# Kernel tuning notes

Measured on AMD Instinct MI355X. Metric: run time of the kernel, lower is better.

Reference implementation:

```python
import jax, jax.numpy as jnp
import numpy as np
import math

H = 2048          # hidden_size
NH = 16           # num_attn_heads
HD = H // NH      # attn head dim = 128
NFW = 4           # num_lact_heads
FD = H // NFW     # fw head dim = 512
DH = FD           # inter_multi = 1.0
CHUNK = 512       # lact_chunk_size
WINDOW = 2048     # window_size
ROPE_BASE = 500000.0
BASE_LR_INV = math.log(math.expm1(0.001))  # inv_softplus(1e-3)


def rmsnorm(x, w, eps=1e-6):
    return x * jax.lax.rsqrt(jnp.mean(x * x, axis=-1, keepdims=True) + eps) * w


def l2norm(x, eps=1e-12):
    return x * jax.lax.rsqrt(jnp.sum(x * x, axis=-1, keepdims=True) + eps)


def rope(x):  # x: [b, h, s, d], half-split convention
    d = x.shape[-1]
    s = x.shape[2]
    inv = 1.0 / (ROPE_BASE ** (jnp.arange(d // 2, dtype=jnp.float32) / (d // 2)))
    f = jnp.arange(s, dtype=jnp.float32)[:, None] * inv[None, :]  # [s, d/2]
    cos, sin = jnp.cos(f), jnp.sin(f)
    x1, x2 = x[..., : d // 2], x[..., d // 2:]
    return jnp.concatenate([x1 * cos - x2 * sin, x2 * cos + x1 * sin], axis=-1)


def setup_inputs() -> dict:
    key = jax.random.key(0)
    ks = jax.random.split(key, 8)
    b, s = 2, 2048
    return {
        "hidden_states": jax.random.normal(ks[0], (b, s, H), jnp.float32),
        "qkv_w": jax.random.normal(ks[1], (3 * H, H), jnp.float32) / math.sqrt(H),
        "q_norm_w": jnp.ones((H,), jnp.float32),
        "k_norm_w": jnp.ones((H,), jnp.float32),
        "qk_scale": jnp.ones((H, 2), jnp.float32),
        "qk_offset": jnp.zeros((H, 2), jnp.float32),
        "lr_w": jax.random.normal(ks[2], (3 * NFW, H), jnp.float32) / math.sqrt(H),
        "lr_b": jnp.zeros((3 * NFW,), jnp.float32),
        "w0": jax.random.normal(ks[3], (NFW, DH, FD), jnp.float32) / math.sqrt(FD),
        "w1": jax.random.normal(ks[4], (NFW, FD, DH), jnp.float32) / math.sqrt(DH),
        "w2": jax.random.normal(ks[5], (NFW, DH, FD), jnp.float32) / math.sqrt(FD),
        "ttt_norm_w": jnp.ones((FD,), jnp.float32),
        "o_proj_w": jax.random.normal(ks[6], (H, H), jnp.float32) / math.sqrt(H),
    }


def reference(hidden_states, qkv_w, q_norm_w, k_norm_w, qk_scale, qk_offset,
              lr_w, lr_b, w0, w1, w2, ttt_norm_w, o_proj_w):
    x = hidden_states
    b, s, _ = x.shape
    nc = s // CHUNK

    qkv = x @ qkv_w.T
    q, k, v = jnp.split(qkv, 3, axis=-1)
    q = rmsnorm(q, q_norm_w)
    k = rmsnorm(k, k_norm_w)

    # ---- TTT (fast-weight SwiGLU) branch ----
    fq = jax.nn.silu(q * qk_scale[:, 0] + qk_offset[:, 0])
    fk = jax.nn.silu(k * qk_scale[:, 1] + qk_offset[:, 1])
    fv = jax.nn.silu(v)
    tohead = lambda t: t.reshape(b, s, NFW, FD).transpose(0, 2, 1, 3)  # [b,h,s,d]
    fq, fk, fv = l2norm(tohead(fq)), l2norm(tohead(fk)), tohead(fv)

    lr = jax.nn.softplus(x @ lr_w.T + lr_b + BASE_LR_INV)          # [b,s,3*NFW]
    lr = lr.reshape(b, s, 3, NFW).transpose(2, 0, 3, 1)[..., None]  # [3,b,h,s,1]
    lr0, lr1, lr2 = lr[0], lr[1], lr[2]

    chunkify = lambda t: t.reshape(b, NFW, nc, CHUNK, -1).transpose(2, 0, 1, 3, 4)
    qs, ks_, vs = chunkify(fq), chunkify(fk), chunkify(fv)
    l0s, l1s, l2s = chunkify(lr0), chunkify(lr1), chunkify(lr2)

    w0b = jnp.broadcast_to(w0, (b,) + w0.shape)
    w1b = jnp.broadcast_to(w1, (b,) + w1.shape)
    w2b = jnp.broadcast_to(w2, (b,) + w2.shape)

    def step(carry, xs):
        w0c, w1c, w2c = carry
        qc, kc, vc, l0, l1, l2 = xs
        # apply current fast weights to queries (strictly causal across chunks)
        hq = jax.nn.silu(jnp.einsum('bhcd,bhed->bhce', qc, w0c)) * \
             jnp.einsum('bhcd,bhed->bhce', qc, w2c)
        oc = jnp.einsum('bhce,bhde->bhcd', hq, w1c)
        # gradient-descent update on dot-product loss -sum(v * f(k))
        g1 = jnp.einsum('bhcd,bhed->bhce', kc, w0c)
        g2 = jnp.einsum('bhcd,bhed->bhce', kc, w2c)
        gate = jax.nn.silu(g1)
        hidden = gate * g2
        dhidden = jnp.einsum('bhcd,bhde->bhce', vc, w1c)  # w1^T v
        dh2 = dhidden * gate
        sig = jax.nn.sigmoid(g1)
        dh1 = dhidden * g2 * (sig * (1.0 + g1 * (1.0 - sig)))  # silu'(g1)
        w1n = w1c + jnp.einsum('bhcd,bhce->bhde', l1 * vc, hidden)
        w0n = w0c + jnp.einsum('bhce,bhcd->bhed', l0 * dh1, kc)
        w2n = w2c + jnp.einsum('bhce,bhcd->bhed', l2 * dh2, kc)
        return (w0n, w1n, w2n), oc

    _, o_chunks = jax.lax.scan(step, (w0b, w1b, w2b), (qs, ks_, vs, l0s, l1s, l2s))
    o_ttt = o_chunks.transpose(1, 2, 0, 3, 4).reshape(b, NFW, s, FD)
    o_ttt = rmsnorm(o_ttt, ttt_norm_w)
    o_ttt = o_ttt.transpose(0, 2, 1, 3).reshape(b, s, H)

    # ---- sliding-window attention branch ----
    qa = rope(q.reshape(b, s, NH, HD).transpose(0, 2, 1, 3))
    ka = rope(k.reshape(b, s, NH, HD).transpose(0, 2, 1, 3))
    va = v.reshape(b, s, NH, HD).transpose(0, 2, 1, 3)
    scores = jnp.einsum('bhqd,bhkd->bhqk', qa, ka) / math.sqrt(HD)
    i = jnp.arange(s)
    mask = (i[:, None] >= i[None, :]) & (i[:, None] - i[None, :] < WINDOW)
    scores = jnp.where(mask, scores, jnp.float32(-1e9))
    p = jax.nn.softmax(scores, axis=-1)
    attn = jnp.einsum('bhqk,bhkd->bhqd', p, va).transpose(0, 2, 1, 3).reshape(b, s, H)

    return (attn + o_ttt) @ o_proj_w.T
```

## Files before the change

kernel.cpp:

```cpp
#include <hip/hip_runtime.h>
#include <hip/hip_bf16.h>
#include <math.h>

using bf16 = __hip_bfloat16;

namespace {

constexpr int cH = 2048;
constexpr int cNH = 16;
constexpr int cHD = 128;
constexpr int cNFW = 4;
constexpr int cFD = 512;
constexpr int cS = 2048;
constexpr float cRSQRT_HD = 0.08838834764831845f;
constexpr long ZL_ = 262144;
constexpr long ZG_ = 1048576;

typedef __attribute__((ext_vector_type(8))) short short8;
typedef __attribute__((ext_vector_type(4))) float f32x4;

__device__ __forceinline__ float sigmoidf_(float x) { return 1.0f / (1.0f + __expf(-x)); }
__device__ __forceinline__ float b2f(bf16 v) { return __bfloat162float(v); }
__device__ __forceinline__ bf16 f2b(float v) { return __float2bfloat16(v); }
__device__ __forceinline__ unsigned short f2bu(float f) {
  return __builtin_bit_cast(unsigned short, __float2bfloat16(f));
}
__device__ __forceinline__ float bu2f(unsigned u) { return __uint_as_float(u << 16); }

#if defined(__has_builtin)
#if __has_builtin(__builtin_amdgcn_global_load_lds)
#define HAVE_GLOAD 1
#endif
#endif

__device__ __forceinline__ void gload16(const bf16* g, short* ldsbase) {
#ifdef HAVE_GLOAD
  __builtin_amdgcn_global_load_lds((const __attribute__((address_space(1))) void*)g,
                                   (__attribute__((address_space(3))) void*)ldsbase, 16, 0, 0);
#else
  const int l = threadIdx.x & 63;
  *(uint4*)(ldsbase + l * 8) = *(const uint4*)g;
#endif
}

__device__ __forceinline__ void stage16(const bf16* src, short* dst) {
  *(uint4*)dst = *(const uint4*)src;
  *(uint4*)(dst + 8) = *(const uint4*)(src + 8);
}

__device__ __forceinline__ void store1(float* p, float v) { *p = v; }
__device__ __forceinline__ void store1(bf16* p, float v) { *p = f2b(v); }

__device__ __forceinline__ void mm_core32(const bf16* __restrict__ Ab, int lda,
                                          const bf16* __restrict__ Bb, int ldb, int K,
                                          short* As, short* Bs, f32x4 acc[4][4]) {
  const int t = threadIdx.x, lane = t & 63, g = lane >> 4, c16 = lane & 15;
  const int wv = t >> 6, wm = (wv >> 1) * 64, wn = (wv & 1) * 64;
  for (int k0 = 0; k0 < K; k0 += 32) {
    __syncthreads();
    {
      const int ch = wv * 2;
      const bf16* ga = Ab + (size_t)(ch * 16 + (lane >> 2)) * lda + k0 + (lane & 3) * 8;
      gload16(ga, &As[ch * 512]);
      gload16(ga + (size_t)16 * lda, &As[ch * 512 + 512]);
      const bf16* gb = Bb + (size_t)(ch * 16 + (lane >> 2)) * ldb + k0 + (lane & 3) * 8;
      gload16(gb, &Bs[ch * 512]);
      gload16(gb + (size_t)16 * ldb, &Bs[ch * 512 + 512]);
    }
    __syncthreads();
    short8 af[4], bfr[4];
#pragma unroll
    for (int mi = 0; mi < 4; ++mi) af[mi] = *(const short8*)&As[(wm + mi * 16 + c16) * 32 + g * 8];
#pragma unroll
    for (int ni = 0; ni < 4; ++ni) bfr[ni] = *(const short8*)&Bs[(wn + ni * 16 + c16) * 32 + g * 8];
#pragma unroll
    for (int mi = 0; mi < 4; ++mi)
#pragma unroll
      for (int ni = 0; ni < 4; ++ni)
        acc[mi][ni] = __builtin_amdgcn_mfma_f32_16x16x32_bf16(af[mi], bfr[ni], acc[mi][ni], 0, 0, 0);
  }
}

template <bool ACC, bool MIR, typename TC>
__device__ __forceinline__ void mm_store(TC* Cb, bf16* Mb, int ldc, int rb, int cb, f32x4 acc[4][4]) {
  const int t = threadIdx.x, lane = t & 63, g = lane >> 4, c16 = lane & 15;
  const int wv = t >> 6, wm = (wv >> 1) * 64, wn = (wv & 1) * 64;
  const int rbase = rb + wm, cbase = cb + wn;
#pragma unroll
  for (int mi = 0; mi < 4; ++mi)
#pragma unroll
    for (int ni = 0; ni < 4; ++ni) {
      const int col = cbase + ni * 16 + c16;
#pragma unroll
      for (int r = 0; r < 4; ++r) {
        const int row = rbase + mi * 16 + g * 4 + r;
        TC* cp = Cb + (size_t)row * ldc + col;
        if constexpr (ACC) {
          float nv = *cp + acc[mi][ni][r];
          *cp = nv;
          if constexpr (MIR) Mb[(size_t)row * ldc + col] = f2b(nv);
        } else {
          store1(cp, acc[mi][ni][r]);
        }
      }
    }
}

template <typename TC>
__global__ __launch_bounds__(256) void k_mm(const bf16* __restrict__ A, int lda,
                                            const bf16* __restrict__ B, int ldb,
                                            TC* __restrict__ C, int ldc, int K) {
  __shared__ short As[128 * 32];
  __shared__ short Bs[128 * 32];
  const bf16* Ab = A + (size_t)blockIdx.y * 128 * lda;
  const bf16* Bb = B + (size_t)blockIdx.x * 128 * ldb;
  f32x4 acc[4][4];
  const f32x4 zero4 = {0.f, 0.f, 0.f, 0.f};
#pragma unroll
  for (int i = 0; i < 4; ++i)
#pragma unroll
    for (int j = 0; j < 4; ++j) acc[i][j] = zero4;
  mm_core32(Ab, lda, Bb, ldb, K, As, Bs, acc);
  mm_store<false, false>(C, (bf16*)nullptr, ldc, blockIdx.y * 128, blockIdx.x * 128, acc);
}

__global__ __launch_bounds__(256) void k_fuse1(const bf16* __restrict__ fq, const bf16* __restrict__ fk,
                                               const bf16* __restrict__ fv,
                                               const bf16* __restrict__ w0b, const bf16* __restrict__ w1t,
                                               const bf16* __restrict__ w2b,
                                               bf16* __restrict__ hq, bf16* __restrict__ trH,
                                               bf16* __restrict__ trD1, bf16* __restrict__ trD2,
                                               bf16* __restrict__ trK, bf16* __restrict__ trV,
                                               const float* __restrict__ lr0, const float* __restrict__ lr1,
                                               const float* __restrict__ lr2,
                                               const bf16* __restrict__ occ,
                                               const float* __restrict__ tw, bf16* __restrict__ y,
                                               int chunk) {
  __shared__ short S[12288];
  __shared__ float red[4];
  const int id = blockIdx.x, t = threadIdx.x;
  const size_t choff = (size_t)chunk * 262144;

  if (id < 512) {
    const int bh = id >> 6, tile = id & 63, by = tile >> 3, bx = tile & 7;
    const int lane = t & 63, g = lane >> 4, c16 = lane & 15, wv = t >> 6;
    const int wm = (wv >> 1) * 32, wn = (wv & 1) * 32;
    const bf16* Aq = fq + (size_t)bh * ZG_ + choff + (size_t)(by * 64) * cFD;
    const bf16* Ak = fk + (size_t)bh * ZG_ + choff + (size_t)(by * 64) * cFD;
    const bf16* Av = fv + (size_t)bh * ZG_ + choff + (size_t)(by * 64) * cFD;
    const bf16* B0 = w0b + (size_t)bh * ZL_ + (size_t)(bx * 64) * cFD;
    const bf16* B2 = w2b + (size_t)bh * ZL_ + (size_t)(bx * 64) * cFD;
    const bf16* B1 = w1t + (size_t)bh * ZL_ + (size_t)(bx * 64) * cFD;

    f32x4 acc[5][2][2];
    const f32x4 zero4 = {0.f, 0.f, 0.f, 0.f};
#pragma unroll
    for (int v = 0; v < 5; ++v)
#pragma unroll
      for (int i = 0; i < 2; ++i)
#pragma unroll
        for (int j = 0; j < 2; ++j) acc[v][i][j] = zero4;

    const int srow = wv * 16 + (lane >> 2), scol = (lane & 3) * 8;
    for (int k0 = 0; k0 < 512; k0 += 32) {
      __syncthreads();
      gload16(Aq + (size_t)srow * cFD + k0 + scol, &S[0 + wv * 512]);
      gload16(Ak + (size_t)srow * cFD + k0 + scol, &S[2048 + wv * 512]);
      gload16(Av + (size_t)srow * cFD + k0 + scol, &S[4096 + wv * 512]);
      gload16(B0 + (size_t)srow * cFD + k0 + scol, &S[6144 + wv * 512]);
      gload16(B2 + (size_t)srow * cFD + k0 + scol, &S[8192 + wv * 512]);
      gload16(B1 + (size_t)srow * cFD + k0 + scol, &S[10240 + wv * 512]);
      __syncthreads();
      short8 aq[2], ak[2], av[2], b0[2], b2[2], b1[2];
#pragma unroll
      for (int mi = 0; mi < 2; ++mi) {
        const int ro = (wm + mi * 16 + c16) * 32 + g * 8;
        aq[mi] = *(const short8*)&S[0 + ro];
        ak[mi] = *(const short8*)&S[2048 + ro];
        av[mi] = *(const short8*)&S[4096 + ro];
      }
#pragma unroll
      for (int ni = 0; ni < 2; ++ni) {
        const int ro = (wn + ni * 16 + c16) * 32 + g * 8;
        b0[ni] = *(const short8*)&S[6144 + ro];
        b2[ni] = *(const short8*)&S[8192 + ro];
        b1[ni] = *(const short8*)&S[10240 + ro];
      }
#pragma unroll
      for (int mi = 0; mi < 2; ++mi)
#pragma unroll
        for (int ni = 0; ni < 2; ++ni) {
          acc[0][mi][ni] = __builtin_amdgcn_mfma_f32_16x16x32_bf16(aq[mi], b0[ni], acc[0][mi][ni], 0, 0, 0);
          acc[1][mi][ni] = __builtin_amdgcn_mfma_f32_16x16x32_bf16(aq[mi], b2[ni], acc[1][mi][ni], 0, 0, 0);
          acc[2][mi][ni] = __builtin_amdgcn_mfma_f32_16x16x32_bf16(ak[mi], b0[ni], acc[2][mi][ni], 0, 0, 0);
          acc[3][mi][ni] = __builtin_amdgcn_mfma_f32_16x16x32_bf16(ak[mi], b2[ni], acc[3][mi][ni], 0, 0, 0);
          acc[4][mi][ni] = __builtin_amdgcn_mfma_f32_16x16x32_bf16(av[mi], b1[ni], acc[4][mi][ni], 0, 0, 0);
        }
    }

    float l0v[2][4], l2v[2][4];
#pragma unroll
    for (int mi = 0; mi < 2; ++mi)
#pragma unroll
      for (int r = 0; r < 4; ++r) {
        const int row = by * 64 + wm + mi * 16 + g * 4 + r;
        l0v[mi][r] = lr0[bh * 2048 + chunk * 512 + row];
        l2v[mi][r] = lr2[bh * 2048 + chunk * 512 + row];
      }
#pragma unroll
    for (int mi = 0; mi < 2; ++mi)
#pragma unroll
      for (int ni = 0; ni < 2; ++ni)
#pragma unroll
        for (int r = 0; r < 4; ++r) {
          float hq1 = acc[0][mi][ni][r], hq2 = acc[1][mi][ni][r];
          float g1 = acc[2][mi][ni][r], g2 = acc[3][mi][ni][r], dh = acc[4][mi][ni][r];
          acc[0][mi][ni][r] = hq1 * sigmoidf_(hq1) * hq2;
          float sg = sigmoidf_(g1);
          float gate = g1 * sg;
          acc[1][mi][ni][r] = gate * g2;
          acc[2][mi][ni][r] = l0v[mi][r] * dh * g2 * (sg * (1.0f + g1 * (1.0f - sg)));
          acc[3][mi][ni][r] = l2v[mi][r] * dh * gate;
        }

    short* Ts = S;
    bf16* dst0 = hq + (size_t)bh * ZL_;
    bf16* dstT[3] = {trH + (size_t)bh * ZL_, trD1 + (size_t)bh * ZL_, trD2 + (size_t)bh * ZL_};
#pragma unroll
    for (int rd = 0; rd < 4; ++rd) {
      __syncthreads();
#pragma unroll
      for (int mi = 0; mi < 2; ++mi)
#pragma unroll
        for (int ni = 0; ni < 2; ++ni)
#pragma unroll
          for (int r = 0; r < 4; ++r) {
            const int row = wm + mi * 16 + g * 4 + r, col = wn + ni * 16 + c16;
            if (rd == 0) Ts[row * 66 + col] = (short)f2bu(acc[0][mi][ni][r]);
            else Ts[col * 66 + row] = (short)f2bu(acc[rd][mi][ni][r]);
          }
      __syncthreads();
      const int rr = t >> 2, cs = (t & 3) * 16;
      unsigned short u[16] __attribute__((aligned(16)));
#pragma unroll
      for (int i = 0; i < 16; ++i) u[i] = (unsigned short)Ts[rr * 66 + cs + i];
      bf16* dp = (rd == 0) ? (dst0 + (size_t)(by * 64 + rr) * cFD + bx * 64 + cs)
                           : (dstT[rd - 1] + (size_t)(bx * 64 + rr) * cFD + by * 64 + cs);
      *(uint4*)dp = *(uint4*)u;
      *(uint4*)(dp + 8) = *(uint4*)(u + 8);
    }
  } else if (id < 1536) {
    short* Ts = S;
    const int id2 = id - 512;
    const int var = id2 >> 9, bh = (id2 >> 6) & 7, by = (id2 >> 3) & 7, bx = id2 & 7;
    const bf16* src = ((var == 0) ? fk : fv) + choff + (size_t)bh * ZG_;
    bf16* dst = ((var == 0) ? trK : trV) + (size_t)bh * ZL_;
    {
      const int rr = t >> 2, cseg = (t & 3) * 16;
      if (var == 0) {
        stage16(src + (size_t)(by * 64 + rr) * cFD + bx * 64 + cseg, &Ts[rr * 72 + cseg]);
      } else {
        const float s = lr1[bh * 2048 + chunk * 512 + by * 64 + rr];
        const bf16* p = src + (size_t)(by * 64 + rr) * cFD + bx * 64 + cseg;
        unsigned short u[16] __attribute__((aligned(16)));
#pragma unroll
        for (int i = 0; i < 16; ++i) u[i] = f2bu(b2f(p[i]) * s);
        *(uint4*)&Ts[rr * 72 + cseg] = *(uint4*)u;
        *(uint4*)&Ts[rr * 72 + cseg + 8] = *(uint4*)(u + 8);
      }
    }
    __syncthreads();
    {
      const int oc_ = t >> 2, rseg = (t & 3) * 16;
      unsigned short u[16] __attribute__((aligned(16)));
#pragma unroll
      for (int i = 0; i < 16; ++i) u[i] = (unsigned short)Ts[(rseg + i) * 72 + oc_];
      bf16* dp = dst + (size_t)(bx * 64 + oc_) * cFD + by * 64 + rseg;
      *(uint4*)dp = *(uint4*)u;
      *(uint4*)(dp + 8) = *(uint4*)(u + 8);
    }
  } else {
    const int rrow = id - 1536;
    const int bh = rrow >> 9, rr = rrow & 511;
    const bf16* src = occ + ((size_t)bh * 512 + rr) * 512;
    float v0 = b2f(src[t]), v1 = b2f(src[t + 256]);
    float ss = v0 * v0 + v1 * v1;
    for (int d = 32; d; d >>= 1) ss += __shfl_down(ss, d);
    if ((t & 63) == 0) red[t >> 6] = ss;
    __syncthreads();
    const float rstd = rsqrtf((red[0] + red[1] + red[2] + red[3]) / cFD + 1e-6f);
    const int si = (chunk - 1) * 512 + rr;
    bf16* dst = y + ((size_t)((bh >> 2) * cS) + si) * cH + (bh & 3) * cFD;
    dst[t] = f2b(b2f(dst[t]) + v0 * rstd * tw[t]);
    dst[t + 256] = f2b(b2f(dst[t + 256]) + v1 * rstd * tw[t + 256]);
  }
}

__global__ __launch_bounds__(256) void k_updna(const bf16* __restrict__ trV, const bf16* __restrict__ trH,
                                               const bf16* __restrict__ trD1, const bf16* __restrict__ trD2,
                                               const bf16* __restrict__ trK,
                                               const bf16* __restrict__ hq, const bf16* __restrict__ w1bc,
                                               float* w0s, float* w1s, float* w2s,
                                               bf16* w0b, bf16* w1bn, bf16* w2b, bf16* w1t,
                                               bf16* __restrict__ occ) {
  __shared__ short Sh[8704];
  const int id = blockIdx.x, t = threadIdx.x;
  const int lane = t & 63, g = lane >> 4, c16 = lane & 15, wv = t >> 6;
  if (id < 384) {
    short* As = Sh;
    short* Bs = Sh + 4096;
    const int z = id >> 4, tile = id & 15, by = tile >> 2, bx = tile & 3;
    const int var = z >> 3, bh = z & 7;
    const bf16 *Aa, *Bb;
    if (var == 0) {
      Aa = trV + (size_t)bh * ZL_ + (size_t)by * 128 * cFD;
      Bb = trH + (size_t)bh * ZL_ + (size_t)bx * 128 * cFD;
    } else if (var == 1) {
      Aa = trD1 + (size_t)bh * ZL_ + (size_t)by * 128 * cFD;
      Bb = trK + (size_t)bh * ZL_ + (size_t)bx * 128 * cFD;
    } else {
      Aa = trD2 + (size_t)bh * ZL_ + (size_t)by * 128 * cFD;
      Bb = trK + (size_t)bh * ZL_ + (size_t)bx * 128 * cFD;
    }
    f32x4 acc[4][4];
    const f32x4 zero4 = {0.f, 0.f, 0.f, 0.f};
#pragma unroll
    for (int i = 0; i < 4; ++i)
#pragma unroll
      for (int j = 0; j < 4; ++j) acc[i][j] = zero4;
    mm_core32(Aa, cFD, Bb, cFD, cFD, As, Bs, acc);
    if (var == 1) {
      mm_store<true, true>(w0s + (size_t)bh * ZL_, w0b + (size_t)bh * ZL_, cFD, by * 128, bx * 128, acc);
    } else if (var == 2) {
      mm_store<true, true>(w2s + (size_t)bh * ZL_, w2b + (size_t)bh * ZL_, cFD, by * 128, bx * 128, acc);
    } else {
      float* W = w1s + (size_t)bh * ZL_;
      bf16* M = w1bn + (size_t)bh * ZL_;
      const int wm = (wv >> 1) * 64, wn = (wv & 1) * 64;
#pragma unroll
      for (int mi = 0; mi < 4; ++mi)
#pragma unroll
        for (int ni = 0; ni < 4; ++ni) {
          const int col = bx * 128 + wn + ni * 16 + c16;
#pragma unroll
          for (int r = 0; r < 4; ++r) {
            const int row = by * 128 + wm + mi * 16 + g * 4 + r;
            float nv = W[(size_t)row * cFD + col] + acc[mi][ni][r];
            W[(size_t)row * cFD + col] = nv;
            M[(size_t)row * cFD + col] = f2b(nv);
            acc[mi][ni][r] = nv;
          }
        }
      bf16* T = w1t + (size_t)bh * ZL_;
      short* Ts = Sh;
#pragma unroll
      for (int rd = 0; rd < 2; ++rd) {
        __syncthreads();
        if (wn == rd * 64) {
#pragma unroll
          for (int mi = 0; mi < 4; ++mi)
#pragma unroll
            for (int ni = 0; ni < 4; ++ni) {
              const int cc = ni * 16 + c16;
              unsigned short u[4] __attribute__((aligned(8)));
#pragma unroll
              for (int r = 0; r < 4; ++r) u[r] = f2bu(acc[mi][ni][r]);
              *(uint2*)&Ts[cc * 136 + wm + mi * 16 + g * 4] = *(uint2*)u;
            }
        }
        __syncthreads();
        const int cc = t >> 2, seg = (t & 3) * 32;
        unsigned short u[32] __attribute__((aligned(16)));
#pragma unroll
        for (int i = 0; i < 32; ++i) u[i] = (unsigned short)Ts[cc * 136 + seg + i];
        bf16* dp = T + (size_t)(bx * 128 + rd * 64 + cc) * cFD + by * 128 + seg;
        *(uint4*)dp = *(uint4*)u;
        *(uint4*)(dp + 8) = *(uint4*)(u + 8);
        *(uint4*)(dp + 16) = *(uint4*)(u + 16);
        *(uint4*)(dp + 24) = *(uint4*)(u + 24);
      }
    }
  } else {
    short* As = Sh;
    short* Bs = Sh + 4096;
    const int id2 = id - 384;
    const int bh = id2 >> 4, tile = id2 & 15, by = tile >> 2, bx = tile & 3;
    const bf16* Aa = hq + (size_t)bh * ZL_ + (size_t)by * 128 * cFD;
    const bf16* Bb = w1bc + (size_t)bh * ZL_ + (size_t)bx * 128 * cFD;
    f32x4 acc[4][4];
    const f32x4 zero4 = {0.f, 0.f, 0.f, 0.f};
#pragma unroll
    for (int i = 0; i < 4; ++i)
#pragma unroll
      for (int j = 0; j < 4; ++j) acc[i][j] = zero4;
    mm_core32(Aa, cFD, Bb, cFD, cFD, As, Bs, acc);
    mm_store<false, false>(occ + (size_t)bh * ZL_, (bf16*)nullptr, cFD, by * 128, bx * 128, acc);
  }
}

__global__ __launch_bounds__(256) void k_normcvt(const bf16* __restrict__ occ,
                                                 const float* __restrict__ tw, bf16* __restrict__ y,
                                                 const float* __restrict__ opw, bf16* __restrict__ opwb,
                                                 int chunk) {
  __shared__ float red[4];
  const int id = blockIdx.x, t = threadIdx.x;
  if (id < 4096) {
    const int bh = id >> 9, rr = id & 511;
    const bf16* src = occ + ((size_t)bh * 512 + rr) * 512;
    float v0 = b2f(src[t]), v1 = b2f(src[t + 256]);
    float ss = v0 * v0 + v1 * v1;
    for (int d = 32; d; d >>= 1) ss += __shfl_down(ss, d);
    if ((t & 63) == 0) red[t >> 6] = ss;
    __syncthreads();
    const float rstd = rsqrtf((red[0] + red[1] + red[2] + red[3]) / cFD + 1e-6f);
    const int si = chunk * 512 + rr;
    bf16* dst = y + ((size_t)((bh >> 2) * cS) + si) * cH + (bh & 3) * cFD;
    dst[t] = f2b(b2f(dst[t]) + v0 * rstd * tw[t]);
    dst[t + 256] = f2b(b2f(dst[t + 256]) + v1 * rstd * tw[t + 256]);
  } else {
    const size_t i = ((size_t)(id - 4096) * 256 + t) * 8;
    float4 a = *(const float4*)(opw + i), b = *(const float4*)(opw + i + 4);
    unsigned short u[8] __attribute__((aligned(16)));
    u[0] = f2bu(a.x); u[1] = f2bu(a.y); u[2] = f2bu(a.z); u[3] = f2bu(a.w);
    u[4] = f2bu(b.x); u[5] = f2bu(b.y); u[6] = f2bu(b.z); u[7] = f2bu(b.w);
    *(uint4*)(opwb + i) = *(uint4*)u;
  }
}

__global__ __launch_bounds__(256) void k_prep(const float* __restrict__ x, const float* __restrict__ qkv_w,
                                              const float* __restrict__ w0, const float* __restrict__ w1,
                                              const float* __restrict__ w2,
                                              const float* __restrict__ lr_w, const float* __restrict__ lr_b,
                                              bf16* __restrict__ xb, bf16* __restrict__ qkvwb,
                                              float* __restrict__ w0s, float* __restrict__ w1s,
                                              float* __restrict__ w2s,
                                              float* __restrict__ ct, float* __restrict__ stb,
                                              float* lr0, float* lr1, float* lr2, float base) {
  __shared__ float xbuf[cH];
  const int id = blockIdx.x, t = threadIdx.x;
  if (id < 4096) {
    const size_t i = ((size_t)id * 256 + t) * 8;
    float4 a = *(const float4*)(x + i), b = *(const float4*)(x + i + 4);
    unsigned short u[8] __attribute__((aligned(16)));
    u[0] = f2bu(a.x); u[1] = f2bu(a.y); u[2] = f2bu(a.z); u[3] = f2bu(a.w);
    u[4] = f2bu(b.x); u[5] = f2bu(b.y); u[6] = f2bu(b.z); u[7] = f2bu(b.w);
    *(uint4*)(xb + i) = *(uint4*)u;
  } else if (id < 10240) {
    const size_t i = ((size_t)(id - 4096) * 256 + t) * 8;
    float4 a = *(const float4*)(qkv_w + i), b = *(const float4*)(qkv_w + i + 4);
    unsigned short u[8] __attribute__((aligned(16)));
    u[0] = f2bu(a.x); u[1] = f2bu(a.y); u[2] = f2bu(a.z); u[3] = f2bu(a.w);
    u[4] = f2bu(b.x); u[5] = f2bu(b.y); u[6] = f2bu(b.z); u[7] = f2bu(b.w);
    *(uint4*)(qkvwb + i) = *(uint4*)u;
  } else if (id < 16384) {
    const int sub = id - 10240;
    const int w = sub >> 11, blk = sub & 2047;
    const size_t i = ((size_t)blk * 256 + t) * 4;
    const int f = (int)((i >> 18) & 3);
    const size_t off = i & 262143;
    const float* src = (w == 0) ? w0 : (w == 1) ? w1 : w2;
    float* dst = (w == 0) ? w0s : (w == 1) ? w1s : w2s;
    *(float4*)(dst + i) = *(const float4*)(src + (size_t)f * 262144 + off);
  } else if (id < 16896) {
    const int gid = (id - 16384) * 256 + t;
    const int si = gid >> 6, jj = gid & 63;
    float inv = powf(500000.0f, -(float)jj / 64.0f);
    float ang = (float)si * inv;
    ct[(size_t)si * 64 + jj] = cosf(ang);
    stb[(size_t)si * 64 + jj] = sinf(ang);
  } else {
    const int token = id - 16896, b_ = token >> 11, si = token & 2047;
    const int wv = t >> 6, lane = t & 63;
    const float* xr = x + (size_t)token * cH;
    for (int i = t; i < cH; i += 256) xbuf[i] = xr[i];
    __syncthreads();
#pragma unroll
    for (int jj = 0; jj < 3; ++jj) {
      const int j = wv * 3 + jj;
      const float* wr = lr_w + (size_t)j * cH;
      float s = 0.f;
      for (int k = lane; k < cH; k += 64) s += xbuf[k] * wr[k];
      for (int d = 32; d; d >>= 1) s += __shfl_down(s, d);
      if (lane == 0) {
        float v = s + lr_b[j] + base;
        float sp = (v > 15.f) ? v : log1pf(expf(v));
        const int tt = j >> 2, f = j & 3;
        float* dst = (tt == 0 ? lr0 : tt == 1 ? lr1 : lr2);
        dst[(size_t)(b_ * cNFW + f) * cS + si] = sp;
      }
    }
  }
}

__global__ __launch_bounds__(256) void k_post2(bf16* __restrict__ qkvh,
                                               const float* __restrict__ qnw, const float* __restrict__ knw,
                                               const float* __restrict__ ct, const float* __restrict__ stb,
                                               bf16* __restrict__ qa, bf16* __restrict__ ka,
                                               bf16* __restrict__ vt) {
  __shared__ short smem[8704];
  __shared__ float red[4];
  const int id = blockIdx.x, t = threadIdx.x;
  if (id < 4096) {
    float* buf = (float*)smem;
    const int token = id, b_ = token >> 11, si = token & 2047;
    bf16* base = qkvh + (size_t)token * 3 * cH;
    for (int pass = 0; pass < 2; ++pass) {
      __syncthreads();
      bf16* src = base + pass * cH;
      const float* nw = pass ? knw : qnw;
      float ss = 0.f;
      for (int i = t; i < cH; i += 256) {
        float v = b2f(src[i]);
        buf[i] = v;
        ss += v * v;
      }
      for (int d = 32; d; d >>= 1) ss += __shfl_down(ss, d);
      if ((t & 63) == 0) red[t >> 6] = ss;
      __syncthreads();
      const float rstd = rsqrtf((red[0] + red[1] + red[2] + red[3]) / cH + 1e-6f);
      for (int i = t; i < cH; i += 256) {
        float v = buf[i] * rstd * nw[i];
        buf[i] = v;
        src[i] = f2b(v);
      }
      __syncthreads();
      bf16* dst = pass ? ka : qa;
      const float scale = pass ? 1.f : cRSQRT_HD;
      const int hh = t >> 4, j0 = (t & 15) * 4;
      const float* cr = ct + (size_t)si * 64 + j0;
      const float* sr = stb + (size_t)si * 64 + j0;
      bf16* drow = dst + ((size_t)(b_ * cNH + hh) * cS + si) * cHD;
      unsigned short u1[4] __attribute__((aligned(8))), u2[4] __attribute__((aligned(8)));
#pragma unroll
      for (int i = 0; i < 4; ++i) {
        float x1 = buf[hh * cHD + j0 + i], x2 = buf[hh * cHD + 64 + j0 + i];
        u1[i] = f2bu((x1 * cr[i] - x2 * sr[i]) * scale);
        u2[i] = f2bu((x2 * cr[i] + x1 * sr[i]) * scale);
      }
      *(uint2*)(drow + j0) = *(uint2*)u1;
      *(uint2*)(drow + 64 + j0) = *(uint2*)u2;
    }
  } else {
    short* Ts = smem;
    const int id2 = id - 4096;
    const int tile = id2 & 31, h = (id2 >> 5) & 15, b_ = id2 >> 9;
    {
      const int r = t >> 2, seg = (t & 3) * 32;
      const bf16* src = qkvh + ((size_t)(b_ * cS) + tile * 64 + r) * 3 * cH + 2 * cH + h * cHD + seg;
      stage16(src, &Ts[r * 136 + seg]);
      stage16(src + 16, &Ts[r * 136 + seg + 16]);
    }
    __syncthreads();
    {
      const int d = t >> 1, seg2 = (t & 1) * 32;
      unsigned short u[32] __attribute__((aligned(16)));
#pragma unroll
      for (int i = 0; i < 32; ++i) u[i] = (unsigned short)Ts[(seg2 + i) * 136 + d];
      bf16* dp = vt + ((size_t)(b_ * cNH + h) * cHD + d) * cS + tile * 64 + seg2;
      *(uint4*)dp = *(uint4*)u;
      *(uint4*)(dp + 8) = *(uint4*)(u + 8);
      *(uint4*)(dp + 16) = *(uint4*)(u + 16);
      *(uint4*)(dp + 24) = *(uint4*)(u + 24);
    }
  }
}

__global__ __launch_bounds__(256) void k_mid(const bf16* __restrict__ qkvh,
                                             const float* __restrict__ qk_scale,
                                             const float* __restrict__ qk_offset,
                                             bf16* fq, bf16* fk, bf16* fv,
                                             const float* __restrict__ w0s_, bf16* __restrict__ w0b_,
                                             const float* __restrict__ w1s_, bf16* __restrict__ w1t_) {
  __shared__ short Ts[64 * 72];
  const int id = blockIdx.x, t = threadIdx.x;
  if (id < 4096) {
    const int token = id, b_ = token >> 11, si = token & 2047;
    const bf16* base = qkvh + (size_t)token * 3 * cH;
#pragma unroll
    for (int pass = 0; pass < 2; ++pass) {
      const bf16* src = base + pass * cH;
      bf16* fdst = pass ? fk : fq;
      const int head = t >> 6, lane = t & 63;
      float f[8];
      float ss2 = 0.f;
#pragma unroll
      for (int k = 0; k < 8; ++k) {
        const int idx = head * cFD + lane + k * 64;
        float v = b2f(src[idx]);
        float u = v * qk_scale[idx * 2 + pass] + qk_offset[idx * 2 + pass];
        float fv_ = u * sigmoidf_(u);
        f[k] = fv_;
        ss2 += fv_ * fv_;
      }
      for (int d = 1; d < 64; d <<= 1) ss2 += __shfl_xor(ss2, d);
      const float sc2 = rsqrtf(ss2 + 1e-12f);
      bf16* dst = fdst + ((size_t)(b_ * cNFW + head) * cS + si) * cFD;
#pragma unroll
      for (int k = 0; k < 8; ++k) dst[lane + k * 64] = f2b(f[k] * sc2);
    }
    const bf16* vr = base + 2 * cH;
    for (int i = t; i < cH; i += 256) {
      float v = b2f(vr[i]);
      fv[((size_t)(b_ * cNFW + (i >> 9)) * cS + si) * cFD + (i & 511)] = f2b(v * sigmoidf_(v));
    }
  } else if (id < 7168) {
    const size_t i = ((size_t)(id - 4096) * 256 + t) * 8;
    float4 a = *(const float4*)(w0s_ + i), b = *(const float4*)(w0s_ + i + 4);
    unsigned short u[8] __attribute__((aligned(16)));
    u[0] = f2bu(a.x); u[1] = f2bu(a.y); u[2] = f2bu(a.z); u[3] = f2bu(a.w);
    u[4] = f2bu(b.x); u[5] = f2bu(b.y); u[6] = f2bu(b.z); u[7] = f2bu(b.w);
    *(uint4*)(w0b_ + i) = *(uint4*)u;
  } else {
    const int id3 = id - 7168;
    const int bh = id3 >> 6, tile = id3 & 63, by = tile >> 3, bx = tile & 7;
    {
      const int rr = t >> 2, cseg = (t & 3) * 16;
      const float* p = w1s_ + (size_t)bh * ZL_ + (size_t)(by * 64 + rr) * cFD + bx * 64 + cseg;
      unsigned short u[16] __attribute__((aligned(16)));
#pragma unroll
      for (int i = 0; i < 16; ++i) u[i] = f2bu(p[i]);
      *(uint4*)&Ts[rr * 72 + cseg] = *(uint4*)u;
      *(uint4*)&Ts[rr * 72 + cseg + 8] = *(uint4*)(u + 8);
    }
    __syncthreads();
    {
      const int oc_ = t >> 2, rseg = (t & 3) * 16;
      unsigned short u[16] __attribute__((aligned(16)));
#pragma unroll
      for (int i = 0; i < 16; ++i) u[i] = (unsigned short)Ts[(rseg + i) * 72 + oc_];
      bf16* dp = w1t_ + (size_t)bh * ZL_ + (size_t)(bx * 64 + oc_) * cFD + by * 64 + rseg;
      *(uint4*)dp = *(uint4*)u;
      *(uint4*)(dp + 8) = *(uint4*)(u + 8);
    }
  }
}

__global__ __launch_bounds__(512) void k_attn6(const bf16* __restrict__ qa, const bf16* __restrict__ ka,
                                               const bf16* __restrict__ vt, bf16* __restrict__ y) {
  const int id = blockIdx.x;
  const int xcd = id & 7;
  const int j = id >> 3;
  const int p = j & 7;
  const int hb = (j >> 3) * 8 + xcd;
  const int h = hb & 15, b_ = hb >> 4;
  __shared__ short KsP[9216];
  __shared__ short Vts[128 * 72];
  const int t = threadIdx.x, lane = t & 63, g = lane >> 4, c16 = lane & 15, wv = t >> 6;
  const size_t hbq = (size_t)(b_ * cNH + h) * cS;
  const bf16* vb = vt + (size_t)(b_ * cNH + h) * (size_t)(cHD * cS);
  const int r = t >> 3, seg = (t & 7) * 16;
  const int dv = t >> 2, seg2 = (t & 3) * 16;
  const f32x4 zero4 = {0.f, 0.f, 0.f, 0.f};

  for (int half = 0; half < 2; ++half) {
    const int qt = half ? p : 15 - p;
    const int q0 = qt * 128;
    const int nkt = 2 * qt + 2;
    short8 qf[4];
    {
      const bf16* qsrc = qa + (hbq + q0 + wv * 16 + c16) * cHD;
#pragma unroll
      for (int ks = 0; ks < 4; ++ks) qf[ks] = *(const short8*)(qsrc + ks * 32 + g * 8);
    }
    f32x4 o[8];
#pragma unroll
    for (int i = 0; i < 8; ++i) o[i] = zero4;
    float m[4], l[4];
#pragma unroll
    for (int rr = 0; rr < 4; ++rr) { m[rr] = -1e30f; l[rr] = 0.f; }

    uint4 kp0, kp1, vp0, vp1;
    {
      const bf16* ksrc = ka + (hbq + r) * cHD + seg;
      kp0 = *(const uint4*)ksrc; kp1 = *(const uint4*)(ksrc + 8);
      const bf16* vsrc = vb + (size_t)dv * cS + seg2;
      vp0 = *(const uint4*)vsrc; vp1 = *(const uint4*)(vsrc + 8);
    }

    for (int kt = 0; kt < nkt; ++kt) {
      __syncthreads();
      {
        short* kd = &KsP[r * 136 + seg];
        *(uint4*)kd = kp0; *(uint4*)(kd + 8) = kp1;
        short* vd = &Vts[dv * 72 + seg2];
        *(uint4*)vd = vp0; *(uint4*)(vd + 8) = vp1;
      }
      __syncthreads();
      if (kt + 1 < nkt) {
        const bf16* ksrc = ka + (hbq + (kt + 1) * 64 + r) * cHD + seg;
        kp0 = *(const uint4*)ksrc; kp1 = *(const uint4*)(ksrc + 8);
        const bf16* vsrc = vb + (size_t)dv * cS + (kt + 1) * 64 + seg2;
        vp0 = *(const uint4*)vsrc; vp1 = *(const uint4*)(vsrc + 8);
      } else if (half == 0) {
        const bf16* ksrc = ka + (hbq + r) * cHD + seg;
        kp0 = *(const uint4*)ksrc; kp1 = *(const uint4*)(ksrc + 8);
        const bf16* vsrc = vb + (size_t)dv * cS + seg2;
        vp0 = *(const uint4*)vsrc; vp1 = *(const uint4*)(vsrc + 8);
      }

      f32x4 s4[4];
#pragma unroll
      for (int ni = 0; ni < 4; ++ni) s4[ni] = zero4;
      __builtin_amdgcn_s_setprio(1);
#pragma unroll
      for (int ks = 0; ks < 4; ++ks) {
#pragma unroll
        for (int ni = 0; ni < 4; ++ni) {
          short8 bb = *(const short8*)&KsP[(ni * 16 + c16) * 136 + ks * 32 + g * 8];
          s4[ni] = __builtin_amdgcn_mfma_f32_16x16x32_bf16(qf[ks], bb, s4[ni], 0, 0, 0);
        }
      }
      __builtin_amdgcn_s_setprio(0);
      __syncthreads();
      if (kt * 64 + 64 > q0) {
#pragma unroll
        for (int ni = 0; ni < 4; ++ni) {
          const int kv = kt * 64 + ni * 16 + c16;
#pragma unroll
          for (int rr = 0; rr < 4; ++rr) {
            const int qr = q0 + wv * 16 + g * 4 + rr;
            if (kv > qr) s4[ni][rr] = -1e9f;
          }
        }
      }
      float mx[4];
#pragma unroll
      for (int rr = 0; rr < 4; ++rr)
        mx[rr] = fmaxf(fmaxf(s4[0][rr], s4[1][rr]), fmaxf(s4[2][rr], s4[3][rr]));
#pragma unroll
      for (int d = 1; d < 16; d <<= 1)
#pragma unroll
        for (int rr = 0; rr < 4; ++rr) mx[rr] = fmaxf(mx[rr], __shfl_xor(mx[rr], d));
      bool need = false;
#pragma unroll
      for (int rr = 0; rr < 4; ++rr) need |= (mx[rr] > m[rr] + 8.f);
      if (__any(need)) {
        float corr[4];
#pragma unroll
        for (int rr = 0; rr < 4; ++rr) {
          float mn = fmaxf(m[rr], mx[rr]);
          corr[rr] = __expf(m[rr] - mn);
          m[rr] = mn;
        }
#pragma unroll
        for (int rr = 0; rr < 4; ++rr) l[rr] *= corr[rr];
#pragma unroll
        for (int nf = 0; nf < 8; ++nf)
#pragma unroll
          for (int rr = 0; rr < 4; ++rr) o[nf][rr] *= corr[rr];
      }
      float psum[4] = {0.f, 0.f, 0.f, 0.f};
#pragma unroll
      for (int ni = 0; ni < 4; ++ni)
#pragma unroll
        for (int rr = 0; rr < 4; ++rr) {
          float pp = __expf(s4[ni][rr] - m[rr]);
          s4[ni][rr] = pp;
          psum[rr] += pp;
        }
#pragma unroll
      for (int d = 1; d < 16; d <<= 1)
#pragma unroll
        for (int rr = 0; rr < 4; ++rr) psum[rr] += __shfl_xor(psum[rr], d);
#pragma unroll
      for (int rr = 0; rr < 4; ++rr) l[rr] += psum[rr];
      short* pw = &KsP[wv * 1152];
#pragma unroll
      for (int ni = 0; ni < 4; ++ni)
#pragma unroll
        for (int rr = 0; rr < 4; ++rr)
          pw[(g * 4 + rr) * 72 + ni * 16 + c16] = (short)f2bu(s4[ni][rr]);
      __builtin_amdgcn_s_setprio(1);
#pragma unroll
      for (int ks2 = 0; ks2 < 2; ++ks2) {
        short8 a = *(const short8*)&pw[c16 * 72 + ks2 * 32 + g * 8];
#pragma unroll
        for (int nf = 0; nf < 8; ++nf) {
          short8 bb = *(const short8*)&Vts[(nf * 16 + c16) * 72 + ks2 * 32 + g * 8];
          o[nf] = __builtin_amdgcn_mfma_f32_16x16x32_bf16(a, bb, o[nf], 0, 0, 0);
        }
      }
      __builtin_amdgcn_s_setprio(0);
    }
    float inv[4];
#pragma unroll
    for (int rr = 0; rr < 4; ++rr) inv[rr] = 1.f / l[rr];
#pragma unroll
    for (int nf = 0; nf < 8; ++nf)
#pragma unroll
      for (int rr = 0; rr < 4; ++rr) {
        const size_t row = (size_t)(b_ * cS) + q0 + wv * 16 + g * 4 + rr;
        y[row * cH + h * cHD + nf * 16 + c16] = f2b(o[nf][rr] * inv[rr]);
      }
  }
}

}

extern "C" void kernel_launch(void* const* d_in, const int* in_sizes, int n_in,
                              void* d_out, int out_size, void* d_ws, size_t ws_size,
                              hipStream_t stream) {
  (void)in_sizes; (void)n_in; (void)out_size; (void)ws_size;
  const float* x         = (const float*)d_in[0];
  const float* qkv_w     = (const float*)d_in[1];
  const float* q_norm_w  = (const float*)d_in[2];
  const float* k_norm_w  = (const float*)d_in[3];
  const float* qk_scale  = (const float*)d_in[4];
  const float* qk_offset = (const float*)d_in[5];
  const float* lr_w      = (const float*)d_in[6];
  const float* lr_b      = (const float*)d_in[7];
  const float* w0        = (const float*)d_in[8];
  const float* w1        = (const float*)d_in[9];
  const float* w2        = (const float*)d_in[10];
  const float* ttt_nw    = (const float*)d_in[11];
  const float* o_proj_w  = (const float*)d_in[12];
  float* out = (float*)d_out;

  char* Wb = (char*)d_ws;
  bf16* qkvh = (bf16*)Wb;
  bf16* hq   = (bf16*)(Wb + 0UL);
  bf16* trH  = (bf16*)(Wb + 4194304UL);
  bf16* trD1 = (bf16*)(Wb + 8388608UL);
  bf16* trD2 = (bf16*)(Wb + 12582912UL);
  bf16* trK  = (bf16*)(Wb + 16777216UL);
  bf16* trV  = (bf16*)(Wb + 20971520UL);
  bf16* occ  = (bf16*)(Wb + 25165824UL);
  bf16* w1t  = (bf16*)(Wb + 29360128UL);
  bf16* w0b  = (bf16*)(Wb + 33554432UL);
  bf16* w1b0 = (bf16*)(Wb + 37748736UL);
  bf16* w2b  = (bf16*)(Wb + 41943040UL);
  bf16* w1b1 = (bf16*)(Wb + 46137344UL);
  bf16* opwb = (bf16*)(Wb + 0UL);
  size_t off = 50331648UL;
  bf16* fqb = (bf16*)(Wb + off); off += 16777216UL;
  bf16* fkb = (bf16*)(Wb + off); off += 16777216UL;
  bf16* fvb = (bf16*)(Wb + off); off += 16777216UL;
  float* w0s = (float*)(Wb + off); off += 8388608UL;
  float* w1s = (float*)(Wb + off); off += 8388608UL;
  float* w2s = (float*)(Wb + off); off += 8388608UL;
  float* lr0 = (float*)(Wb + off); off += 65536UL;
  float* lr1 = (float*)(Wb + off); off += 65536UL;
  float* lr2 = (float*)(Wb + off); off += 65536UL;
  bf16* y = (bf16*)(Wb + off); off += 16777216UL;
  float* ct  = (float*)(Wb + off); off += 524288UL;
  float* stb = (float*)(Wb + off); off += 524288UL;
  bf16* xb = fqb;
  bf16* qkvwb = fkb;
  bf16* qa = fqb;
  bf16* ka = fkb;
  bf16* vt = fvb;
  bf16* w1m[2] = {w1b0, w1b1};

  const float base_lr_inv = logf(expm1f(0.001f));
  dim3 blk(256);

  k_prep<<<dim3(20992), blk, 0, stream>>>(x, qkv_w, w0, w1, w2, lr_w, lr_b,
                                          xb, qkvwb, w0s, w1s, w2s, ct, stb,
                                          lr0, lr1, lr2, base_lr_inv);
  k_mm<bf16><<<dim3(48, 32), blk, 0, stream>>>(xb, 2048, qkvwb, 2048, qkvh, 6144, 2048);
  k_post2<<<dim3(5120), blk, 0, stream>>>(qkvh, q_norm_w, k_norm_w, ct, stb, qa, ka, vt);
  k_attn6<<<dim3(256), dim3(512), 0, stream>>>(qa, ka, vt, y);
  k_mid<<<dim3(7680), blk, 0, stream>>>(qkvh, qk_scale, qk_offset, fqb, fkb, fvb,
                                        w0s, w0b, w1s, w1t);

  for (int c = 0; c < 4; ++c) {
    const int g1 = (c == 0) ? 1536 : 5632;
    k_fuse1<<<dim3(g1), blk, 0, stream>>>(fqb, fkb, fvb, w0b, w1t, w2b,
                                          hq, trH, trD1, trD2, trK, trV,
                                          lr0, lr1, lr2, occ, ttt_nw, y, c);
    k_updna<<<dim3(512), blk, 0, stream>>>(trV, trH, trD1, trD2, trK, hq, w1m[c & 1],
                                           w0s, w1s, w2s, w0b, w1m[(c + 1) & 1], w2b, w1t,
                                           occ);
  }
  k_normcvt<<<dim3(6144), blk, 0, stream>>>(occ, ttt_nw, y, o_proj_w, opwb, 3);
  k_mm<float><<<dim3(16, 32), blk, 0, stream>>>(y, 2048, opwb, 2048, out, 2048, 2048);
}
```

Measured before the change: 696.4 us.

## Replace GEMM kernel with 256x128 tiled, double-buffered 8-wave MFMA kernel

Replaces the 128x128 single-buffered GEMM used for the QKV and output projections with a 512-thread kernel computing 256x128 tiles. It uses K=64 steps, double-buffered LDS, direct global-to-LDS loads interleaved with MFMA, barriers split per half-tile, and raised wave priority during the MFMA sections. The aim is to hide memory latency and raise per-block data reuse. In exchange it halves the block count (768 and 256 blocks), which may underfill the GPU for the smaller output projection, and the schedule depends on hand-placed waitcnts being correct.

```diff
diff --git a/kernel.cpp b/kernel.cpp
--- a/kernel.cpp
+++ b/kernel.cpp
@@ -107,21 +107,104 @@
 }
 
 template <typename TC>
-__global__ __launch_bounds__(256) void k_mm(const bf16* __restrict__ A, int lda,
-                                            const bf16* __restrict__ B, int ldb,
-                                            TC* __restrict__ C, int ldc, int K) {
-  __shared__ short As[128 * 32];
-  __shared__ short Bs[128 * 32];
-  const bf16* Ab = A + (size_t)blockIdx.y * 128 * lda;
+__global__ __launch_bounds__(512, 1) void k_mm8(const bf16* __restrict__ A, int lda,
+                                                const bf16* __restrict__ B, int ldb,
+                                                TC* __restrict__ C, int ldc, int K) {
+  __shared__ short LA[2][256 * 64];
+  __shared__ short LB[2][128 * 64];
+  const int t = threadIdx.x, lane = t & 63, wv = t >> 6;
+  const int g = lane >> 4, c16 = lane & 15;
+  const int wm = (wv >> 1) * 64, wn = (wv & 1) * 64;
+  const bf16* Ab = A + (size_t)blockIdx.y * 256 * lda;
   const bf16* Bb = B + (size_t)blockIdx.x * 128 * ldb;
+  const int NKT = K >> 6;
+  const int srow = wv * 16 + (lane >> 3), scol = (lane & 7) * 8;
+
+  auto stA = [&](int buf, int half, int kt) {
+    const int ktc = (kt < NKT) ? kt : 0;
+    const bf16* src = Ab + (size_t)(half * 128 + srow) * lda + ktc * 64 + scol;
+    short* dst = &LA[buf][(half * 128 + wv * 16) * 64];
+    gload16(src, dst);
+    gload16(src + (size_t)8 * lda, dst + 512);
+  };
+  auto stB = [&](int buf, int kt) {
+    const int ktc = (kt < NKT) ? kt : 0;
+    const bf16* src = Bb + (size_t)srow * ldb + ktc * 64 + scol;
+    short* dst = &LB[buf][(wv * 16) * 64];
+    gload16(src, dst);
+    gload16(src + (size_t)8 * ldb, dst + 512);
+  };
+
   f32x4 acc[4][4];
   const f32x4 zero4 = {0.f, 0.f, 0.f, 0.f};
 #pragma unroll
   for (int i = 0; i < 4; ++i)
 #pragma unroll
     for (int j = 0; j < 4; ++j) acc[i][j] = zero4;
-  mm_core32(Ab, lda, Bb, ldb, K, As, Bs, acc);
-  mm_store<false, false>(C, (bf16*)nullptr, ldc, blockIdx.y * 128, blockIdx.x * 128, acc);
+
+  stB(0, 0);
+  stA(0, 0, 0);
+  stA(0, 1, 0);
+  stB(1, 1);
+  asm volatile("s_waitcnt vmcnt(0)" ::: "memory");
+  __syncthreads();
+
+  const int NITER = NKT >> 1;
+  for (int it = 0; it < NITER; ++it) {
+    const int T = 2 * it;
+#pragma unroll
+    for (int hf = 0; hf < 2; ++hf) {
+      short8 bfr[4][2];
+#pragma unroll
+      for (int p = 0; p < 2; ++p) {
+        if (p == 0) {
+#pragma unroll
+          for (int ni = 0; ni < 4; ++ni)
+#pragma unroll
+            for (int kk = 0; kk < 2; ++kk)
+              bfr[ni][kk] = *(const short8*)&LB[hf][(wn + ni * 16 + c16) * 64 + kk * 32 + g * 8];
+        }
+        short8 af[2][2];
+#pragma unroll
+        for (int j = 0; j < 2; ++j)
+#pragma unroll
+          for (int kk = 0; kk < 2; ++kk)
+            af[j][kk] = *(const short8*)&LA[hf][(wm + (p * 2 + j) * 16 + c16) * 64 + kk * 32 + g * 8];
+        if (p == 0) {
+          stA(hf ^ 1, 0, T + 1 + hf);
+        } else {
+          stA(hf ^ 1, 1, T + 1 + hf);
+          stB(hf, T + 2 + hf);
+        }
+        asm volatile("" ::: "memory");
+        __builtin_amdgcn_s_barrier();
+        __builtin_amdgcn_s_setprio(1);
+#pragma unroll
+        for (int j = 0; j < 2; ++j)
+#pragma unroll
+          for (int ni = 0; ni < 4; ++ni)
+#pragma unroll
+            for (int kk = 0; kk < 2; ++kk)
+              acc[p * 2 + j][ni] = __builtin_amdgcn_mfma_f32_16x16x32_bf16(
+                  af[j][kk], bfr[ni][kk], acc[p * 2 + j][ni], 0, 0, 0);
+        __builtin_amdgcn_s_setprio(0);
+        if (p == 1) asm volatile("s_waitcnt vmcnt(2)" ::: "memory");
+        asm volatile("" ::: "memory");
+        __builtin_amdgcn_s_barrier();
+      }
+    }
+  }
+
+  const int rbase = blockIdx.y * 256 + wm, cbase = blockIdx.x * 128 + wn;
+#pragma unroll
+  for (int fr = 0; fr < 4; ++fr)
+#pragma unroll
+    for (int ni = 0; ni < 4; ++ni) {
+      const int col = cbase + ni * 16 + c16;
+#pragma unroll
+      for (int r = 0; r < 4; ++r)
+        store1(C + (size_t)(rbase + fr * 16 + g * 4 + r) * ldc + col, acc[fr][ni][r]);
+    }
 }
 
 __global__ __launch_bounds__(256) void k_fuse1(const bf16* __restrict__ fq, const bf16* __restrict__ fk,
@@ -857,7 +940,7 @@
   k_prep<<<dim3(20992), blk, 0, stream>>>(x, qkv_w, w0, w1, w2, lr_w, lr_b,
                                           xb, qkvwb, w0s, w1s, w2s, ct, stb,
                                           lr0, lr1, lr2, base_lr_inv);
-  k_mm<bf16><<<dim3(48, 32), blk, 0, stream>>>(xb, 2048, qkvwb, 2048, qkvh, 6144, 2048);
+  k_mm8<bf16><<<dim3(48, 16), dim3(512), 0, stream>>>(xb, 2048, qkvwb, 2048, qkvh, 6144, 2048);
   k_post2<<<dim3(5120), blk, 0, stream>>>(qkvh, q_norm_w, k_norm_w, ct, stb, qa, ka, vt);
   k_attn6<<<dim3(256), dim3(512), 0, stream>>>(qa, ka, vt, y);
   k_mid<<<dim3(7680), blk, 0, stream>>>(qkvh, qk_scale, qk_offset, fqb, fkb, fvb,
@@ -873,5 +956,5 @@
                                            occ);
   }
   k_normcvt<<<dim3(6144), blk, 0, stream>>>(occ, ttt_nw, y, o_proj_w, opwb, 3);
-  k_mm<float><<<dim3(16, 32), blk, 0, stream>>>(y, 2048, opwb, 2048, out, 2048, 2048);
-}
+  k_mm8<float><<<dim3(16, 16), dim3(512), 0, stream>>>(y, 2048, opwb, 2048, out, 2048, 2048);
+}
```

Result: slower. 734.6 us (+5.5%).
